# Performance work log

Measured on AMD Instinct MI355X. Metric: run time of the kernel, lower is better.

The kernel has to match this reference:

```python
import jax, jax.numpy as jnp
import numpy as np

EPS = 1e-8
NUM_HEADS = 4


def setup_inputs() -> dict:
    key = jax.random.key(0)
    ks = jax.random.split(key, 20)
    N, D = 8192, 200      # total nodes, gnn/text dim
    B = 4                  # graphs (text batch)
    E, DEG = 4096, 16      # hyperedges, nodes per hyperedge
    H = 128                # fusion hidden dim
    f = lambda k, s: jax.random.normal(k, s, dtype=jnp.float32) * 0.05
    return {
        "x": jax.random.normal(ks[0], (N, D), dtype=jnp.float32),
        "text": jax.random.normal(ks[1], (B, D), dtype=jnp.float32),
        "W": f(ks[2], (D, D)),
        "b": jnp.zeros((D,), jnp.float32),
        "gate_w": f(ks[3], (D, 1)),
        "gate_b": jnp.zeros((1,), jnp.float32),
        "gnn_w": f(ks[4], (D, H)), "gnn_b": f(ks[5], (H,)),
        "text_w": f(ks[6], (D, H)), "text_b": f(ks[7], (H,)),
        "in_w": f(ks[8], (H, 3 * H)), "in_b": f(ks[9], (3 * H,)),
        "attn_out_w": f(ks[10], (H, H)), "attn_out_b": f(ks[11], (H,)),
        "fgate_w": f(ks[12], (2 * H, H)), "fgate_b": f(ks[13], (H,)),
        "outp_w": f(ks[14], (H, D)), "outp_b": f(ks[15], (D,)),
        "edge_nodes": jax.random.randint(ks[16], (E, DEG), 0, N),
    }


def _forward(x, text, W, b, gate_w, gate_b, gnn_w, gnn_b, text_w, text_b,
             in_w, in_b, attn_out_w, attn_out_b, fgate_w, fgate_b,
             outp_w, outp_b, edge_nodes):
    N, D = x.shape
    E, DEG = edge_nodes.shape
    # --- HypergraphConv: incidence build + normalized Laplacian propagation ---
    out = x @ W                                         # [N, D]
    # H[node, edge] = 1/len(edge); duplicates overwrite (set), as in torch loop
    Hinc = jnp.zeros((N, E), x.dtype).at[edge_nodes, jnp.arange(E)[:, None]].set(1.0 / DEG)
    Dv = Hinc.sum(axis=1)                               # node degree [N]
    De = Hinc.sum(axis=0)                               # edge degree [E]
    dv = 1.0 / jnp.sqrt(Dv + EPS)
    de = 1.0 / (De + EPS)
    Hl = Hinc * dv[:, None]                             # Dv^-1/2 H
    L = (Hl * de[None, :]) @ Hl.T                       # Dv^-1/2 H De^-1 H^T Dv^-1/2
    hyper_out = L @ out                                 # [N, D]
    alpha = jax.nn.sigmoid(x.mean(axis=0, keepdims=True) @ gate_w + gate_b)  # [1,1]
    gnn_feat = alpha * out + (1.0 - alpha) * hyper_out + b
    # --- CrossModalAttentionFusion on per-graph node features (3D path) ---
    B = text.shape[0]
    Nn = N // B
    gnn3 = gnn_feat.reshape(B, Nn, D)
    gp = gnn3 @ gnn_w + gnn_b                           # [B, Nn, H]
    tp = (text @ text_w + text_b)[:, None, :]           # [B, 1, H]
    Hd = gp.shape[-1]
    hd = Hd // NUM_HEADS
    q = gp @ in_w[:, :Hd] + in_b[:Hd]
    k = tp @ in_w[:, Hd:2 * Hd] + in_b[Hd:2 * Hd]
    v = tp @ in_w[:, 2 * Hd:] + in_b[2 * Hd:]
    qh = q.reshape(B, Nn, NUM_HEADS, hd).transpose(0, 2, 1, 3)   # [B,h,Nn,hd]
    kh = k.reshape(B, 1, NUM_HEADS, hd).transpose(0, 2, 1, 3)    # [B,h,1,hd]
    vh = v.reshape(B, 1, NUM_HEADS, hd).transpose(0, 2, 1, 3)
    scores = jnp.einsum("bhqd,bhkd->bhqk", qh, kh) / jnp.sqrt(jnp.float32(hd))
    attn = jax.nn.softmax(scores, axis=-1)              # kv_len=1 -> ones
    att = jnp.einsum("bhqk,bhkd->bhqd", attn, vh)
    att = att.transpose(0, 2, 1, 3).reshape(B, Nn, Hd) @ attn_out_w + attn_out_b
    g = jax.nn.sigmoid(jnp.concatenate([gp, att], axis=-1) @ fgate_w + fgate_b)
    fused = g * gp + (1.0 - g) * att
    return fused @ outp_w + outp_b                      # [B, Nn, D]


def reference(x, text, W, b, gate_w, gate_b, gnn_w, gnn_b, text_w, text_b,
              in_w, in_b, attn_out_w, attn_out_b, fgate_w, fgate_b,
              outp_w, outp_b, edge_nodes):
    return _forward(x, text, W, b, gate_w, gate_b, gnn_w, gnn_b, text_w, text_b,
                    in_w, in_b, attn_out_w, attn_out_b, fgate_w, fgate_b,
                    outp_w, outp_b, edge_nodes)
```

## Files before the change

kernel.cpp:

```cpp
#include <hip/hip_runtime.h>

#define NODES 8192
#define DIM   200
#define NEDGE 4096
#define DEGREE 16
#define HD    128
#define MT    8
#define ECAP  32

__device__ __forceinline__ float dv_of(int cnt) {
    return 1.0f / sqrtf((float)cnt * (1.0f / 16.0f) + 1e-8f);
}

__global__ void k_front(const float* __restrict__ x, const float* __restrict__ W,
                        const float* __restrict__ gnn_w, const float* __restrict__ bias,
                        const float* __restrict__ gnn_b, const float* __restrict__ text,
                        const float* __restrict__ text_w, const float* __restrict__ text_b,
                        const float* __restrict__ in_w, const float* __restrict__ in_b,
                        const float* __restrict__ aow, const float* __restrict__ aob,
                        const float* __restrict__ fgw, const float* __restrict__ fgb,
                        float* __restrict__ cpart, int* __restrict__ cnt,
                        float* __restrict__ Wg, float* __restrict__ bg,
                        float* __restrict__ attO, float* __restrict__ attg) {
    __shared__ float st[DIM];
    __shared__ float part[2][HD];
    __shared__ float vin[HD];
    int b = blockIdx.x, t = threadIdx.x;
    if (b < 256) {
        if (t < 32) cnt[b * 32 + t] = 0;
        if (t < DIM) {
            float acc = 0.f;
            int r0 = b * 32;
            for (int r = 0; r < 32; r++) acc += x[(r0 + r) * DIM + t];
            cpart[b * DIM + t] = acc;
        }
        return;
    }
    if (b < 356) {
        int r = 2 * (b - 256) + (t >> 7);
        int c = t & 127;
        const float* vec = &W[r * DIM];
        float acc = 0.f;
        for (int k = 0; k < DIM; k++) acc += vec[k] * gnn_w[k * HD + c];
        Wg[r * HD + c] = acc;
        return;
    }
    if (b == 356) {
        if (t < HD) {
            float acc = 0.f;
            for (int k = 0; k < DIM; k++) acc += bias[k] * gnn_w[k * HD + t];
            bg[t] = acc + gnn_b[t];
        }
        return;
    }
    int g = b - 357;
    int c = t & 127, h = t >> 7;
    if (t < DIM) st[t] = text[g * DIM + t];
    __syncthreads();
    {
        float acc = 0.f;
        int k0 = h * 100;
        for (int k = k0; k < k0 + 100; k++) acc += st[k] * text_w[k * HD + c];
        part[h][c] = acc;
    }
    __syncthreads();
    if (t < HD) vin[t] = part[0][t] + part[1][t] + text_b[t];
    __syncthreads();
    {
        float acc = 0.f;
        int k0 = h * 64;
        for (int k = k0; k < k0 + 64; k++) acc += vin[k] * in_w[k * 3 * HD + 2 * HD + c];
        part[h][c] = acc;
    }
    __syncthreads();
    if (t < HD) vin[t] = part[0][t] + part[1][t] + in_b[2 * HD + t];
    __syncthreads();
    {
        float acc = 0.f;
        int k0 = h * 64;
        for (int k = k0; k < k0 + 64; k++) acc += vin[k] * aow[k * HD + c];
        part[h][c] = acc;
    }
    __syncthreads();
    if (t < HD) {
        float ao = part[0][t] + part[1][t] + aob[t];
        attO[g * HD + t] = ao;
        vin[t] = ao;
    }
    __syncthreads();
    {
        float acc = 0.f;
        int k0 = h * 64;
        for (int k = k0; k < k0 + 64; k++) acc += vin[k] * fgw[(HD + k) * HD + c];
        part[h][c] = acc;
    }
    __syncthreads();
    if (t < HD) attg[g * HD + t] = part[0][t] + part[1][t] + fgb[t];
}

__global__ void k_xwg(const float* __restrict__ x, const float* __restrict__ Wg,
                      const int* __restrict__ en, float* __restrict__ out2,
                      int* __restrict__ cnt, int* __restrict__ emask,
                      int* __restrict__ elist2, const float* __restrict__ cpart,
                      const float* __restrict__ gate_w, const float* __restrict__ gate_b,
                      float* __restrict__ alpha) {
    __shared__ float sx[16 * DIM];
    int t = threadIdx.x;
    if (blockIdx.x == 512) {
        __shared__ float red[256];
        float v = 0.f;
        if (t < DIM) {
            float s = 0.f;
            for (int q = 0; q < 256; q++) s += cpart[q * DIM + t];
            v = s * gate_w[t];
        }
        red[t] = v;
        __syncthreads();
        for (int o = 128; o > 0; o >>= 1) {
            if (t < o) red[t] += red[t + o];
            __syncthreads();
        }
        if (t == 0) {
            float z = red[0] / (float)NODES + gate_b[0];
            alpha[0] = 1.0f / (1.0f + expf(-z));
        }
        return;
    }
    int b = blockIdx.x;
    if (t < 8) {
        int e = b * 8 + t;
        int idx[DEGREE];
#pragma unroll
        for (int i = 0; i < DEGREE; i++) idx[i] = en[e * DEGREE + i];
        int mask = 0;
#pragma unroll
        for (int i = 0; i < DEGREE; i++) {
            bool uniq = true;
            for (int j = 0; j < i; j++) uniq = uniq && (idx[j] != idx[i]);
            if (uniq) {
                mask |= (1 << i);
                int slot = atomicAdd(&cnt[idx[i]], 1);
                if (slot < ECAP) elist2[idx[i] * ECAP + slot] = e;
            }
        }
        emask[e] = mask;
    }
    int bm = b * 16;
    const float4* x4 = (const float4*)(x + bm * DIM);
    float4* sx4 = (float4*)sx;
    for (int i = t; i < 16 * DIM / 4; i += 256) sx4[i] = x4[i];
    __syncthreads();
    int rg = t >> 6;
    int c0 = t & 63;
    float acc[4][2] = {{0.f,0.f},{0.f,0.f},{0.f,0.f},{0.f,0.f}};
    for (int k = 0; k < DIM; k++) {
        float w0 = Wg[k * HD + c0];
        float w1 = Wg[k * HD + c0 + 64];
#pragma unroll
        for (int i = 0; i < 4; i++) {
            float s = sx[(rg * 4 + i) * DIM + k];
            acc[i][0] += s * w0;
            acc[i][1] += s * w1;
        }
    }
#pragma unroll
    for (int i = 0; i < 4; i++) {
        out2[(bm + rg * 4 + i) * HD + c0]      = acc[i][0];
        out2[(bm + rg * 4 + i) * HD + c0 + 64] = acc[i][1];
    }
}

__global__ void k_tE(const int* __restrict__ en, const int* __restrict__ emask,
                     const int* __restrict__ cnt, const float* __restrict__ out2,
                     float* __restrict__ tE) {
    int e = blockIdx.x * 2 + (threadIdx.x >> 7);
    int c = threadIdx.x & 127;
    int m = emask[e];
    float De = (float)__popc(m) * (1.0f / 16.0f);
    float de = 1.0f / (De + 1e-8f);
    int nd[DEGREE];
#pragma unroll
    for (int i = 0; i < DEGREE; i++) nd[i] = en[e * DEGREE + i];
    float acc = 0.f;
#pragma unroll
    for (int i = 0; i < DEGREE; i++)
        if ((m >> i) & 1) acc += dv_of(cnt[nd[i]]) * out2[nd[i] * HD + c];
    tE[e * HD + c] = de * acc;
}

__global__ void k_tail(const float* __restrict__ out2, const float* __restrict__ tE,
                       const int* __restrict__ cnt, const int* __restrict__ elist2,
                       const float* __restrict__ alpha, const float* __restrict__ bg,
                       const float* __restrict__ fgw, const float* __restrict__ attO,
                       const float* __restrict__ attg, const float* __restrict__ opw,
                       const float* __restrict__ opb, float* __restrict__ out) {
    __shared__ float sgp[MT][HD];
    __shared__ int   sid[MT][ECAP];
    __shared__ int   scount[MT];
    int bm = blockIdx.x * MT;
    int b = bm >> 11;
    int t = threadIdx.x;
    {
        int r = t >> 5, sl = t & 31;
        int n = bm + r;
        int cc = cnt[n]; cc = cc < ECAP ? cc : ECAP;
        if (sl == 0) scount[r] = cc;
        if (sl < cc) sid[r][sl] = elist2[n * ECAP + sl];
    }
    __syncthreads();
    int c = t & 127, rg = t >> 7;
    float a = alpha[0];
    float bgc = bg[c];
#pragma unroll
    for (int i = 0; i < 4; i++) {
        int r = rg * 4 + i;
        int n = bm + r;
        int cc = scount[r];
        float hyp = 0.f;
        for (int j = 0; j < cc; j++) hyp += tE[sid[r][j] * HD + c];
        hyp *= dv_of(cnt[n]) * (1.0f / 256.0f);
        sgp[r][c] = a * out2[n * HD + c] + (1.0f - a) * hyp + bgc;
    }
    __syncthreads();
    float ao = attO[b * HD + c];
    float ag = attg[b * HD + c];
    float acc[4] = {ag, ag, ag, ag};
    for (int j = 0; j < HD; j++) {
        float w = fgw[j * HD + c];
#pragma unroll
        for (int i = 0; i < 4; i++) acc[i] += sgp[rg * 4 + i][j] * w;
    }
    __syncthreads();
#pragma unroll
    for (int i = 0; i < 4; i++) {
        int r = rg * 4 + i;
        float g = 1.0f / (1.0f + expf(-acc[i]));
        sgp[r][c] = g * sgp[r][c] + (1.0f - g) * ao;
    }
    __syncthreads();
    if (t < DIM) {
        float accO[MT];
        float ob = opb[t];
#pragma unroll
        for (int i = 0; i < MT; i++) accO[i] = ob;
        for (int j = 0; j < HD; j++) {
            float w = opw[j * DIM + t];
#pragma unroll
            for (int i = 0; i < MT; i++) accO[i] += sgp[i][j] * w;
        }
#pragma unroll
        for (int i = 0; i < MT; i++) out[(bm + i) * DIM + t] = accO[i];
    }
}

extern "C" void kernel_launch(void* const* d_in, const int* in_sizes, int n_in,
                              void* d_out, int out_size, void* d_ws, size_t ws_size,
                              hipStream_t stream) {
    const float* x      = (const float*)d_in[0];
    const float* text   = (const float*)d_in[1];
    const float* W      = (const float*)d_in[2];
    const float* bias   = (const float*)d_in[3];
    const float* gate_w = (const float*)d_in[4];
    const float* gate_b = (const float*)d_in[5];
    const float* gnn_w  = (const float*)d_in[6];
    const float* gnn_b  = (const float*)d_in[7];
    const float* text_w = (const float*)d_in[8];
    const float* text_b = (const float*)d_in[9];
    const float* in_w   = (const float*)d_in[10];
    const float* in_b   = (const float*)d_in[11];
    const float* aow    = (const float*)d_in[12];
    const float* aob    = (const float*)d_in[13];
    const float* fgw    = (const float*)d_in[14];
    const float* fgb    = (const float*)d_in[15];
    const float* opw    = (const float*)d_in[16];
    const float* opb    = (const float*)d_in[17];
    const int*   en     = (const int*)d_in[18];
    float* out = (float*)d_out;

    char* q = (char*)d_ws;
    int*   cnt    = (int*)q;   q += NODES * sizeof(int);
    float* cpart  = (float*)q; q += 256 * DIM * sizeof(float);
    float* out2   = (float*)q; q += (size_t)NODES * HD * sizeof(float);
    float* tE     = (float*)q; q += (size_t)NEDGE * HD * sizeof(float);
    int*   elist2 = (int*)q;   q += (size_t)NODES * ECAP * sizeof(int);
    float* Wg     = (float*)q; q += DIM * HD * sizeof(float);
    float* alpha  = (float*)q; q += sizeof(float);
    float* bg     = (float*)q; q += HD * sizeof(float);
    float* attO   = (float*)q; q += 4 * HD * sizeof(float);
    float* attg   = (float*)q; q += 4 * HD * sizeof(float);
    int*   emask  = (int*)q;   q += NEDGE * sizeof(int);

    k_front<<<361, 256, 0, stream>>>(x, W, gnn_w, bias, gnn_b, text, text_w, text_b,
                                     in_w, in_b, aow, aob, fgw, fgb,
                                     cpart, cnt, Wg, bg, attO, attg);
    k_xwg<<<513, 256, 0, stream>>>(x, Wg, en, out2, cnt, emask, elist2,
                                   cpart, gate_w, gate_b, alpha);
    k_tE<<<NEDGE / 2, 256, 0, stream>>>(en, emask, cnt, out2, tE);
    k_tail<<<NODES / MT, 256, 0, stream>>>(out2, tE, cnt, elist2, alpha, bg, fgw,
                                           attO, attg, opw, opb, out);
}
```

Baseline: 160.9 us.

## Fuse column-sum into xwg tile load, move alpha to k_tE, widen tail tiles

The per-column sum of x now comes from the 16-row tile k_xwg already stages in shared memory, so k_front no longer reads x a second time. The alpha gate reduction moves into an extra block of k_tE, which sums twice as many partials. k_tail now processes 16 nodes per block and unrolls its hyperedge gather to a fixed 16 slots to expose memory-level parallelism, with a slow path when a node has more than 16 edges. In exchange, k_tail holds more registers per thread and issues some wasted loads for padded slots, and the dependency edges between kernels shift.

```diff
diff --git a/kernel.cpp b/kernel.cpp
--- a/kernel.cpp
+++ b/kernel.cpp
@@ -5,39 +5,33 @@
 #define NEDGE 4096
 #define DEGREE 16
 #define HD    128
-#define MT    8
+#define MT    16
 #define ECAP  32
+#define CPB   512
 
 __device__ __forceinline__ float dv_of(int cnt) {
     return 1.0f / sqrtf((float)cnt * (1.0f / 16.0f) + 1e-8f);
 }
 
-__global__ void k_front(const float* __restrict__ x, const float* __restrict__ W,
-                        const float* __restrict__ gnn_w, const float* __restrict__ bias,
-                        const float* __restrict__ gnn_b, const float* __restrict__ text,
-                        const float* __restrict__ text_w, const float* __restrict__ text_b,
-                        const float* __restrict__ in_w, const float* __restrict__ in_b,
-                        const float* __restrict__ aow, const float* __restrict__ aob,
-                        const float* __restrict__ fgw, const float* __restrict__ fgb,
-                        float* __restrict__ cpart, int* __restrict__ cnt,
+__global__ void k_front(const float* __restrict__ W, const float* __restrict__ gnn_w,
+                        const float* __restrict__ bias, const float* __restrict__ gnn_b,
+                        const float* __restrict__ text, const float* __restrict__ text_w,
+                        const float* __restrict__ text_b, const float* __restrict__ in_w,
+                        const float* __restrict__ in_b, const float* __restrict__ aow,
+                        const float* __restrict__ aob, const float* __restrict__ fgw,
+                        const float* __restrict__ fgb, int* __restrict__ cnt,
                         float* __restrict__ Wg, float* __restrict__ bg,
                         float* __restrict__ attO, float* __restrict__ attg) {
     __shared__ float st[DIM];
     __shared__ float part[2][HD];
     __shared__ float vin[HD];
     int b = blockIdx.x, t = threadIdx.x;
-    if (b < 256) {
-        if (t < 32) cnt[b * 32 + t] = 0;
-        if (t < DIM) {
-            float acc = 0.f;
-            int r0 = b * 32;
-            for (int r = 0; r < 32; r++) acc += x[(r0 + r) * DIM + t];
-            cpart[b * DIM + t] = acc;
-        }
+    if (b < 32) {
+        cnt[b * 256 + t] = 0;
         return;
     }
-    if (b < 356) {
-        int r = 2 * (b - 256) + (t >> 7);
+    if (b < 132) {
+        int r = 2 * (b - 32) + (t >> 7);
         int c = t & 127;
         const float* vec = &W[r * DIM];
         float acc = 0.f;
@@ -45,7 +39,7 @@
         Wg[r * HD + c] = acc;
         return;
     }
-    if (b == 356) {
+    if (b == 132) {
         if (t < HD) {
             float acc = 0.f;
             for (int k = 0; k < DIM; k++) acc += bias[k] * gnn_w[k * HD + t];
@@ -53,7 +47,7 @@
         }
         return;
     }
-    int g = b - 357;
+    int g = b - 133;
     int c = t & 127, h = t >> 7;
     if (t < DIM) st[t] = text[g * DIM + t];
     __syncthreads();
@@ -101,32 +95,38 @@
 __global__ void k_xwg(const float* __restrict__ x, const float* __restrict__ Wg,
                       const int* __restrict__ en, float* __restrict__ out2,
                       int* __restrict__ cnt, int* __restrict__ emask,
-                      int* __restrict__ elist2, const float* __restrict__ cpart,
-                      const float* __restrict__ gate_w, const float* __restrict__ gate_b,
-                      float* __restrict__ alpha) {
+                      int* __restrict__ elist2, float* __restrict__ cpart) {
     __shared__ float sx[16 * DIM];
-    int t = threadIdx.x;
-    if (blockIdx.x == 512) {
-        __shared__ float red[256];
-        float v = 0.f;
-        if (t < DIM) {
-            float s = 0.f;
-            for (int q = 0; q < 256; q++) s += cpart[q * DIM + t];
-            v = s * gate_w[t];
-        }
-        red[t] = v;
-        __syncthreads();
-        for (int o = 128; o > 0; o >>= 1) {
-            if (t < o) red[t] += red[t + o];
-            __syncthreads();
-        }
-        if (t == 0) {
-            float z = red[0] / (float)NODES + gate_b[0];
-            alpha[0] = 1.0f / (1.0f + expf(-z));
-        }
-        return;
-    }
-    int b = blockIdx.x;
+    int b = blockIdx.x, t = threadIdx.x;
+    int bm = b * 16;
+    const float4* x4 = (const float4*)(x + bm * DIM);
+    float4* sx4 = (float4*)sx;
+    for (int i = t; i < 16 * DIM / 4; i += 256) sx4[i] = x4[i];
+    __syncthreads();
+    if (t < DIM) {
+        float s = 0.f;
+#pragma unroll
+        for (int r = 0; r < 16; r++) s += sx[r * DIM + t];
+        cpart[b * DIM + t] = s;
+    }
+    int rg = t >> 6;
+    int c0 = t & 63;
+    float acc[4][2] = {{0.f,0.f},{0.f,0.f},{0.f,0.f},{0.f,0.f}};
+    for (int k = 0; k < DIM; k++) {
+        float w0 = Wg[k * HD + c0];
+        float w1 = Wg[k * HD + c0 + 64];
+#pragma unroll
+        for (int i = 0; i < 4; i++) {
+            float s = sx[(rg * 4 + i) * DIM + k];
+            acc[i][0] += s * w0;
+            acc[i][1] += s * w1;
+        }
+    }
+#pragma unroll
+    for (int i = 0; i < 4; i++) {
+        out2[(bm + rg * 4 + i) * HD + c0]      = acc[i][0];
+        out2[(bm + rg * 4 + i) * HD + c0 + 64] = acc[i][1];
+    }
     if (t < 8) {
         int e = b * 8 + t;
         int idx[DEGREE];
@@ -145,36 +145,36 @@
         }
         emask[e] = mask;
     }
-    int bm = b * 16;
-    const float4* x4 = (const float4*)(x + bm * DIM);
-    float4* sx4 = (float4*)sx;
-    for (int i = t; i < 16 * DIM / 4; i += 256) sx4[i] = x4[i];
-    __syncthreads();
-    int rg = t >> 6;
-    int c0 = t & 63;
-    float acc[4][2] = {{0.f,0.f},{0.f,0.f},{0.f,0.f},{0.f,0.f}};
-    for (int k = 0; k < DIM; k++) {
-        float w0 = Wg[k * HD + c0];
-        float w1 = Wg[k * HD + c0 + 64];
-#pragma unroll
-        for (int i = 0; i < 4; i++) {
-            float s = sx[(rg * 4 + i) * DIM + k];
-            acc[i][0] += s * w0;
-            acc[i][1] += s * w1;
-        }
-    }
-#pragma unroll
-    for (int i = 0; i < 4; i++) {
-        out2[(bm + rg * 4 + i) * HD + c0]      = acc[i][0];
-        out2[(bm + rg * 4 + i) * HD + c0 + 64] = acc[i][1];
-    }
 }
 
 __global__ void k_tE(const int* __restrict__ en, const int* __restrict__ emask,
                      const int* __restrict__ cnt, const float* __restrict__ out2,
-                     float* __restrict__ tE) {
-    int e = blockIdx.x * 2 + (threadIdx.x >> 7);
-    int c = threadIdx.x & 127;
+                     float* __restrict__ tE, const float* __restrict__ cpart,
+                     const float* __restrict__ gate_w, const float* __restrict__ gate_b,
+                     float* __restrict__ alpha) {
+    int t = threadIdx.x;
+    if (blockIdx.x == NEDGE / 2) {
+        __shared__ float red[256];
+        float v = 0.f;
+        if (t < DIM) {
+            float s = 0.f;
+            for (int q = 0; q < CPB; q++) s += cpart[q * DIM + t];
+            v = s * gate_w[t];
+        }
+        red[t] = v;
+        __syncthreads();
+        for (int o = 128; o > 0; o >>= 1) {
+            if (t < o) red[t] += red[t + o];
+            __syncthreads();
+        }
+        if (t == 0) {
+            float z = red[0] / (float)NODES + gate_b[0];
+            alpha[0] = 1.0f / (1.0f + expf(-z));
+        }
+        return;
+    }
+    int e = blockIdx.x * 2 + (t >> 7);
+    int c = t & 127;
     int m = emask[e];
     float De = (float)__popc(m) * (1.0f / 16.0f);
     float de = 1.0f / (De + 1e-8f);
@@ -195,45 +195,55 @@
                        const float* __restrict__ attg, const float* __restrict__ opw,
                        const float* __restrict__ opb, float* __restrict__ out) {
     __shared__ float sgp[MT][HD];
-    __shared__ int   sid[MT][ECAP];
+    __shared__ int   sid[MT][16];
     __shared__ int   scount[MT];
     int bm = blockIdx.x * MT;
-    int b = bm >> 11;
+    int gb = bm >> 11;
     int t = threadIdx.x;
     {
-        int r = t >> 5, sl = t & 31;
+        int r = t >> 4, sl = t & 15;
         int n = bm + r;
         int cc = cnt[n]; cc = cc < ECAP ? cc : ECAP;
         if (sl == 0) scount[r] = cc;
-        if (sl < cc) sid[r][sl] = elist2[n * ECAP + sl];
+        int ccs = cc < 16 ? cc : 16;
+        sid[r][sl] = (sl < ccs) ? elist2[n * ECAP + sl] : 0;
     }
     __syncthreads();
     int c = t & 127, rg = t >> 7;
     float a = alpha[0];
     float bgc = bg[c];
 #pragma unroll
-    for (int i = 0; i < 4; i++) {
-        int r = rg * 4 + i;
+    for (int i = 0; i < 8; i++) {
+        int r = rg * 8 + i;
         int n = bm + r;
         int cc = scount[r];
+        int ccs = cc < 16 ? cc : 16;
         float hyp = 0.f;
-        for (int j = 0; j < cc; j++) hyp += tE[sid[r][j] * HD + c];
+#pragma unroll
+        for (int j = 0; j < 16; j++) {
+            float v = tE[sid[r][j] * HD + c];
+            hyp += (j < ccs) ? v : 0.f;
+        }
+        if (cc > 16)
+            for (int j = 16; j < cc; j++) hyp += tE[elist2[n * ECAP + j] * HD + c];
         hyp *= dv_of(cnt[n]) * (1.0f / 256.0f);
         sgp[r][c] = a * out2[n * HD + c] + (1.0f - a) * hyp + bgc;
     }
     __syncthreads();
-    float ao = attO[b * HD + c];
-    float ag = attg[b * HD + c];
-    float acc[4] = {ag, ag, ag, ag};
+    float ao = attO[gb * HD + c];
+    float ag = attg[gb * HD + c];
+    float acc[8];
+#pragma unroll
+    for (int i = 0; i < 8; i++) acc[i] = ag;
     for (int j = 0; j < HD; j++) {
         float w = fgw[j * HD + c];
 #pragma unroll
-        for (int i = 0; i < 4; i++) acc[i] += sgp[rg * 4 + i][j] * w;
-    }
-    __syncthreads();
-#pragma unroll
-    for (int i = 0; i < 4; i++) {
-        int r = rg * 4 + i;
+        for (int i = 0; i < 8; i++) acc[i] += sgp[rg * 8 + i][j] * w;
+    }
+    __syncthreads();
+#pragma unroll
+    for (int i = 0; i < 8; i++) {
+        int r = rg * 8 + i;
         float g = 1.0f / (1.0f + expf(-acc[i]));
         sgp[r][c] = g * sgp[r][c] + (1.0f - g) * ao;
     }
@@ -279,7 +289,7 @@
 
     char* q = (char*)d_ws;
     int*   cnt    = (int*)q;   q += NODES * sizeof(int);
-    float* cpart  = (float*)q; q += 256 * DIM * sizeof(float);
+    float* cpart  = (float*)q; q += (size_t)CPB * DIM * sizeof(float);
     float* out2   = (float*)q; q += (size_t)NODES * HD * sizeof(float);
     float* tE     = (float*)q; q += (size_t)NEDGE * HD * sizeof(float);
     int*   elist2 = (int*)q;   q += (size_t)NODES * ECAP * sizeof(int);
@@ -290,12 +300,12 @@
     float* attg   = (float*)q; q += 4 * HD * sizeof(float);
     int*   emask  = (int*)q;   q += NEDGE * sizeof(int);
 
-    k_front<<<361, 256, 0, stream>>>(x, W, gnn_w, bias, gnn_b, text, text_w, text_b,
+    k_front<<<137, 256, 0, stream>>>(W, gnn_w, bias, gnn_b, text, text_w, text_b,
                                      in_w, in_b, aow, aob, fgw, fgb,
-                                     cpart, cnt, Wg, bg, attO, attg);
-    k_xwg<<<513, 256, 0, stream>>>(x, Wg, en, out2, cnt, emask, elist2,
-                                   cpart, gate_w, gate_b, alpha);
-    k_tE<<<NEDGE / 2, 256, 0, stream>>>(en, emask, cnt, out2, tE);
+                                     cnt, Wg, bg, attO, attg);
+    k_xwg<<<512, 256, 0, stream>>>(x, Wg, en, out2, cnt, emask, elist2, cpart);
+    k_tE<<<NEDGE / 2 + 1, 256, 0, stream>>>(en, emask, cnt, out2, tE,
+                                            cpart, gate_w, gate_b, alpha);
     k_tail<<<NODES / MT, 256, 0, stream>>>(out2, tE, cnt, elist2, alpha, bg, fgw,
                                            attO, attg, opw, opb, out);
 }
```

Measured after the change: 174.4 us. 1.08x slower.
